# Performance work log

Hardware: AMD Instinct MI355X
Metric: run time of the kernel (lower is better)

Reference implementation:

```python
import jax, jax.numpy as jnp
import numpy as np

N_NODES = 50000
HIDDEN = 64
N_EDGES = 1200000


def setup_inputs() -> dict:
    key = jax.random.key(0)
    ks = jax.random.split(key, 12)
    x = jax.random.normal(ks[0], (N_NODES, HIDDEN), dtype=jnp.float32)
    edge_index = jax.random.randint(ks[1], (2, N_EDGES), 0, N_NODES, dtype=jnp.int64)
    s = 1.0 / np.sqrt(HIDDEN)
    # RGCN layer (single relation): relation weight, root weight, bias
    W_rel1 = jax.random.normal(ks[2], (HIDDEN, HIDDEN), dtype=jnp.float32) * s
    W_root1 = jax.random.normal(ks[3], (HIDDEN, HIDDEN), dtype=jnp.float32) * s
    b1 = jnp.zeros((HIDDEN,), dtype=jnp.float32)
    # Three GraphConv layers: self weight, neighbor weight, bias each
    W_self2 = jax.random.normal(ks[4], (HIDDEN, HIDDEN), dtype=jnp.float32) * s
    W_nbr2 = jax.random.normal(ks[5], (HIDDEN, HIDDEN), dtype=jnp.float32) * s
    b2 = jnp.zeros((HIDDEN,), dtype=jnp.float32)
    W_self3 = jax.random.normal(ks[6], (HIDDEN, HIDDEN), dtype=jnp.float32) * s
    W_nbr3 = jax.random.normal(ks[7], (HIDDEN, HIDDEN), dtype=jnp.float32) * s
    b3 = jnp.zeros((HIDDEN,), dtype=jnp.float32)
    W_self4 = jax.random.normal(ks[8], (HIDDEN, HIDDEN), dtype=jnp.float32) * s
    W_nbr4 = jax.random.normal(ks[9], (HIDDEN, HIDDEN), dtype=jnp.float32) * s
    b4 = jnp.zeros((HIDDEN,), dtype=jnp.float32)
    return {
        "x": x, "edge_index": edge_index,
        "W_rel1": W_rel1, "W_root1": W_root1, "b1": b1,
        "W_self2": W_self2, "W_nbr2": W_nbr2, "b2": b2,
        "W_self3": W_self3, "W_nbr3": W_nbr3, "b3": b3,
        "W_self4": W_self4, "W_nbr4": W_nbr4, "b4": b4,
    }


def _rgcn(x, W_rel, W_root, b, src, dst, n_nodes):
    # single-relation RGCN: root transform + mean-aggregated relation transform
    msg = x[src] @ W_rel                                   # [E, H]
    agg = jax.ops.segment_sum(msg, dst, num_segments=n_nodes)
    cnt = jax.ops.segment_sum(jnp.ones((src.shape[0],), x.dtype), dst, num_segments=n_nodes)
    agg = agg / jnp.maximum(cnt, 1.0)[:, None]
    return x @ W_root + agg + b


def _graphconv(x, W_self, W_nbr, b, src, dst, n_nodes):
    # GraphConv: self transform + sum-aggregated neighbor transform
    agg = jax.ops.segment_sum(x[src], dst, num_segments=n_nodes)  # [N, H]
    return x @ W_self + agg @ W_nbr + b


def reference(x, edge_index, W_rel1, W_root1, b1, W_self2, W_nbr2, b2,
              W_self3, W_nbr3, b3, W_self4, W_nbr4, b4):
    n = x.shape[0]
    src, dst = edge_index[0], edge_index[1]
    h = jax.nn.relu(_rgcn(x, W_rel1, W_root1, b1, src, dst, n))
    h = jax.nn.relu(_graphconv(h, W_self2, W_nbr2, b2, src, dst, n))
    x_1 = h
    h = jax.nn.relu(_graphconv(h, W_self3, W_nbr3, b3, src, dst, n))
    h = jax.nn.relu(_graphconv(h, W_self4, W_nbr4, b4, src, dst, n))
    x_2 = h
    return (x_1, x_2)
```

## Files before the change

kernel.cpp:

```cpp
#include <hip/hip_runtime.h>

#define N_NODES 50000
#define HIDDEN  64
#define N_EDGES 1200000

#define BSHIFT 8
#define NBUK   196
#define GBIN   256
#define PAD    8192

__device__ __forceinline__ float bcastf(float v, int k) {
    return __int_as_float(__builtin_amdgcn_readlane(__float_as_int(v), k));
}

__device__ __forceinline__ unsigned short f2bf(float x) {
    unsigned u = __float_as_uint(x);
    u += 0x7fffu + ((u >> 16) & 1u);
    return (unsigned short)(u >> 16);
}

__device__ __forceinline__ float bfl(unsigned w) { return __uint_as_float(w << 16); }
__device__ __forceinline__ float bfh(unsigned w) { return __uint_as_float(w & 0xffff0000u); }


__global__ void init_kernel(int* __restrict__ cursor) {
    int tid = threadIdx.x;
    if (tid < NBUK) cursor[tid] = tid * PAD;
}

__global__ __launch_bounds__(256) void scatter_fused_kernel(const int* __restrict__ ei,
                                                            int* __restrict__ cursor,
                                                            int2* __restrict__ tmp, int E) {
    __shared__ int h[NBUK];
    __shared__ int cur[NBUK];
    int tid = threadIdx.x;
    if (tid < NBUK) h[tid] = 0;
    __syncthreads();
    for (int e = blockIdx.x * 256 + tid; e < E; e += GBIN * 256)
        atomicAdd(&h[ei[E + e] >> BSHIFT], 1);
    __syncthreads();
    if (tid < NBUK) cur[tid] = atomicAdd(&cursor[tid], h[tid]);
    __syncthreads();
    for (int e = blockIdx.x * 256 + tid; e < E; e += GBIN * 256) {
        int src = ei[e];
        int dst = ei[E + e];
        int p = atomicAdd(&cur[dst >> BSHIFT], 1);
        tmp[p] = make_int2(src, dst);
    }
}

__global__ __launch_bounds__(256) void bucketize_kernel(const int2* __restrict__ tmp,
                                                        const int* __restrict__ cursor,
                                                        int2* __restrict__ row_info,
                                                        int* __restrict__ csr_src, int n) {
    __shared__ int hist[256];
    __shared__ int cur[256];
    __shared__ int stage[PAD];
    int b = blockIdx.x, tid = threadIdx.x;
    int base = b * PAD;
    int count = cursor[b] - base;
    int node_base = b << BSHIFT;

    hist[tid] = 0;
    __syncthreads();
    for (int i = tid; i < count; i += 256)
        atomicAdd(&hist[tmp[base + i].y - node_base], 1);
    __syncthreads();
    int v = hist[tid];
#pragma unroll
    for (int o = 1; o < 256; o <<= 1) {
        __syncthreads();
        int y = (tid >= o) ? hist[tid - o] : 0;
        __syncthreads();
        hist[tid] += y;
    }
    __syncthreads();
    int excl = hist[tid] - v;
    cur[tid] = excl;
    int node = node_base + tid;
    if (node < n) row_info[node] = make_int2(base + excl, v);
    __syncthreads();
    for (int i = tid; i < count; i += 256) {
        int2 p = tmp[base + i];
        int slot = atomicAdd(&cur[p.y - node_base], 1);
        stage[slot] = p.x;
    }
    __syncthreads();
    for (int i = tid; i < count; i += 256)
        csr_src[base + i] = stage[i];
}

__global__ __launch_bounds__(256) void gemm2_kernel(const float* __restrict__ h,
                                                    const float* __restrict__ Wnbr,
                                                    const float* __restrict__ Wself,
                                                    const float* __restrict__ bias,
                                                    unsigned short* __restrict__ tbf,
                                                    float* __restrict__ u, int n) {
    int lane = threadIdx.x & 63;
    float wn[64], ws[64];
#pragma unroll
    for (int k = 0; k < 64; ++k) {
        wn[k] = Wnbr[k * 64 + lane];
        ws[k] = Wself[k * 64 + lane];
    }
    float bv = bias[lane];
    int wave = (blockIdx.x * 256 + threadIdx.x) >> 6;
    int nwaves = gridDim.x * 4;
    if (wave == 0) tbf[(size_t)n * 64 + lane] = 0;
    for (int i = wave; i < n; i += nwaves) {
        float hv = h[i * 64 + lane];
        float tacc = 0.f, uacc = bv;
#pragma unroll
        for (int k = 0; k < 64; ++k) {
            float hk = bcastf(hv, k);
            tacc = fmaf(hk, wn[k], tacc);
            uacc = fmaf(hk, ws[k], uacc);
        }
        tbf[(size_t)i * 64 + lane] = f2bf(tacc);
        u[(size_t)i * 64 + lane] = uacc;
    }
}

__global__ __launch_bounds__(256) void agg_kernel(const unsigned short* __restrict__ tbf,
                                                  const float* __restrict__ u,
                                                  const int2* __restrict__ row_info,
                                                  const int* __restrict__ csr_src,
                                                  float* __restrict__ out, int n, int use_mean) {
    int lane = threadIdx.x & 63;
    int g = lane >> 4;
    int q = lane & 15;
    int node = (blockIdx.x * 256 + threadIdx.x) >> 6;
    if (node >= n) return;
    int2 ri = row_info[node];
    int start = ri.x, deg = ri.y;
    float4 a0 = {0,0,0,0}, a1 = {0,0,0,0}, a2 = {0,0,0,0}, a3 = {0,0,0,0};
    for (int e = 0; e < deg; e += 64) {
        int cnt = deg - e;
        if (cnt > 64) cnt = 64;
        int idx = (lane < cnt) ? csr_src[start + e + lane] : n;
        int cnt16 = (cnt + 15) & ~15;
        for (int j = 0; j < cnt16; j += 16) {
            int s0 = __shfl(idx, j + g);
            int s1 = __shfl(idx, j + 4 + g);
            int s2 = __shfl(idx, j + 8 + g);
            int s3 = __shfl(idx, j + 12 + g);
            const uint2 w0 = *(const uint2*)(tbf + (size_t)s0 * 64 + q * 4);
            const uint2 w1 = *(const uint2*)(tbf + (size_t)s1 * 64 + q * 4);
            const uint2 w2 = *(const uint2*)(tbf + (size_t)s2 * 64 + q * 4);
            const uint2 w3 = *(const uint2*)(tbf + (size_t)s3 * 64 + q * 4);
            a0.x += bfl(w0.x); a0.y += bfh(w0.x); a0.z += bfl(w0.y); a0.w += bfh(w0.y);
            a1.x += bfl(w1.x); a1.y += bfh(w1.x); a1.z += bfl(w1.y); a1.w += bfh(w1.y);
            a2.x += bfl(w2.x); a2.y += bfh(w2.x); a2.z += bfl(w2.y); a2.w += bfh(w2.y);
            a3.x += bfl(w3.x); a3.y += bfh(w3.x); a3.z += bfl(w3.y); a3.w += bfh(w3.y);
        }
    }
    float4 acc;
    acc.x = (a0.x + a1.x) + (a2.x + a3.x);
    acc.y = (a0.y + a1.y) + (a2.y + a3.y);
    acc.z = (a0.z + a1.z) + (a2.z + a3.z);
    acc.w = (a0.w + a1.w) + (a2.w + a3.w);
    acc.x += __shfl_xor(acc.x, 16); acc.y += __shfl_xor(acc.y, 16);
    acc.z += __shfl_xor(acc.z, 16); acc.w += __shfl_xor(acc.w, 16);
    acc.x += __shfl_xor(acc.x, 32); acc.y += __shfl_xor(acc.y, 32);
    acc.z += __shfl_xor(acc.z, 32); acc.w += __shfl_xor(acc.w, 32);

    float scale = 1.f;
    if (use_mean) scale = 1.f / fmaxf((float)deg, 1.f);
    if (g == 0) {
        const float4 uv = *(const float4*)(u + (size_t)node * 64 + q * 4);
        float4 r;
        r.x = fmaxf(uv.x + acc.x * scale, 0.f);
        r.y = fmaxf(uv.y + acc.y * scale, 0.f);
        r.z = fmaxf(uv.z + acc.z * scale, 0.f);
        r.w = fmaxf(uv.w + acc.w * scale, 0.f);
        *(float4*)(out + (size_t)node * 64 + q * 4) = r;
    }
}


extern "C" void kernel_launch(void* const* d_in, const int* in_sizes, int n_in,
                              void* d_out, int out_size, void* d_ws, size_t ws_size,
                              hipStream_t stream) {
    const float* x      = (const float*)d_in[0];
    const int*   ei     = (const int*)d_in[1];
    const float* Wrel1  = (const float*)d_in[2];
    const float* Wroot1 = (const float*)d_in[3];
    const float* b1     = (const float*)d_in[4];
    const float* Wself2 = (const float*)d_in[5];
    const float* Wnbr2  = (const float*)d_in[6];
    const float* b2     = (const float*)d_in[7];
    const float* Wself3 = (const float*)d_in[8];
    const float* Wnbr3  = (const float*)d_in[9];
    const float* b3     = (const float*)d_in[10];
    const float* Wself4 = (const float*)d_in[11];
    const float* Wnbr4  = (const float*)d_in[12];
    const float* b4     = (const float*)d_in[13];

    const int N = N_NODES, E = N_EDGES;

    auto align = [](size_t o) { return (o + 255) & ~(size_t)255; };
    char* base = (char*)d_ws;
    size_t off = 0;
    int*  cursor   = (int*)(base + off);  off = align(off + 256 * 4);
    int2* row_info = (int2*)(base + off); off = align(off + (size_t)N * 8);
    int*  csr_src  = (int*)(base + off);  off = align(off + (size_t)NBUK * PAD * 4);
    int2* tmp      = (int2*)(base + off); off = align(off + (size_t)NBUK * PAD * 8);
    unsigned short* tbf = (unsigned short*)(base + off); off = align(off + (size_t)(N + 1) * 64 * 2);
    float* u  = (float*)(base + off); off = align(off + (size_t)N * 64 * 4);
    float* h1 = (float*)(base + off); off = align(off + (size_t)N * 64 * 4);

    float* out1 = (float*)d_out;
    float* out2 = (float*)d_out + (size_t)N * 64;

    init_kernel<<<1, 256, 0, stream>>>(cursor);
    scatter_fused_kernel<<<GBIN, 256, 0, stream>>>(ei, cursor, tmp, E);
    bucketize_kernel<<<NBUK, 256, 0, stream>>>(tmp, cursor, row_info, csr_src, N);

    const int GB = 768;
    const int AB = (N + 3) / 4;

    gemm2_kernel<<<GB, 256, 0, stream>>>(x, Wrel1, Wroot1, b1, tbf, u, N);
    agg_kernel<<<AB, 256, 0, stream>>>(tbf, u, row_info, csr_src, h1, N, 1);
    gemm2_kernel<<<GB, 256, 0, stream>>>(h1, Wnbr2, Wself2, b2, tbf, u, N);
    agg_kernel<<<AB, 256, 0, stream>>>(tbf, u, row_info, csr_src, out1, N, 0);
    gemm2_kernel<<<GB, 256, 0, stream>>>(out1, Wnbr3, Wself3, b3, tbf, u, N);
    agg_kernel<<<AB, 256, 0, stream>>>(tbf, u, row_info, csr_src, h1, N, 0);
    gemm2_kernel<<<GB, 256, 0, stream>>>(h1, Wnbr4, Wself4, b4, tbf, u, N);
    agg_kernel<<<AB, 256, 0, stream>>>(tbf, u, row_info, csr_src, out2, N, 0);
}
```

Measured before the change: 326.4 us.

## Compress CSR indices to 16-bit, shrink buckets, widen aggregation unroll

The edge binning now packs each source index and its bucket-local destination into one 32-bit word, and stores the final CSR source indices as 16-bit values. Buckets shrink to 128 nodes and are processed by 512-thread blocks. The aggregation kernel doubles its gather unroll from 4 to 8 neighbour rows per step, using 8 accumulators. The aims are to cut memory traffic in the preprocessing and index reads and to keep more gathers in flight per wave. In exchange, correctness depends on node ids fitting in 16 bits and on each bucket holding no more than 4096 edges.

Measured after the change: 336.1 us. 1.03x slower.

```diff
diff --git a/kernel.cpp b/kernel.cpp
--- a/kernel.cpp
+++ b/kernel.cpp
@@ -4,10 +4,11 @@
 #define HIDDEN  64
 #define N_EDGES 1200000
 
-#define BSHIFT 8
-#define NBUK   196
+#define BSHIFT 7
+#define BUKSZ  128
+#define NBUK   391
 #define GBIN   256
-#define PAD    8192
+#define PAD2   4096
 
 __device__ __forceinline__ float bcastf(float v, int k) {
     return __int_as_float(__builtin_amdgcn_readlane(__float_as_int(v), k));
@@ -23,71 +24,74 @@
 __device__ __forceinline__ float bfh(unsigned w) { return __uint_as_float(w & 0xffff0000u); }
 
 
-__global__ void init_kernel(int* __restrict__ cursor) {
+__global__ __launch_bounds__(512) void init_kernel(int* __restrict__ cursor) {
     int tid = threadIdx.x;
-    if (tid < NBUK) cursor[tid] = tid * PAD;
+    if (tid < NBUK) cursor[tid] = tid * PAD2;
 }
 
 __global__ __launch_bounds__(256) void scatter_fused_kernel(const int* __restrict__ ei,
                                                             int* __restrict__ cursor,
-                                                            int2* __restrict__ tmp, int E) {
+                                                            int* __restrict__ tmp, int E) {
     __shared__ int h[NBUK];
     __shared__ int cur[NBUK];
     int tid = threadIdx.x;
-    if (tid < NBUK) h[tid] = 0;
+    for (int b = tid; b < NBUK; b += 256) h[b] = 0;
     __syncthreads();
     for (int e = blockIdx.x * 256 + tid; e < E; e += GBIN * 256)
         atomicAdd(&h[ei[E + e] >> BSHIFT], 1);
     __syncthreads();
-    if (tid < NBUK) cur[tid] = atomicAdd(&cursor[tid], h[tid]);
+    for (int b = tid; b < NBUK; b += 256) cur[b] = atomicAdd(&cursor[b], h[b]);
     __syncthreads();
     for (int e = blockIdx.x * 256 + tid; e < E; e += GBIN * 256) {
         int src = ei[e];
         int dst = ei[E + e];
         int p = atomicAdd(&cur[dst >> BSHIFT], 1);
-        tmp[p] = make_int2(src, dst);
-    }
-}
-
-__global__ __launch_bounds__(256) void bucketize_kernel(const int2* __restrict__ tmp,
+        tmp[p] = src | ((dst & (BUKSZ - 1)) << 16);
+    }
+}
+
+__global__ __launch_bounds__(512) void bucketize_kernel(const int* __restrict__ tmp,
                                                         const int* __restrict__ cursor,
                                                         int2* __restrict__ row_info,
-                                                        int* __restrict__ csr_src, int n) {
-    __shared__ int hist[256];
-    __shared__ int cur[256];
-    __shared__ int stage[PAD];
+                                                        unsigned short* __restrict__ csr,
+                                                        int n) {
+    __shared__ int hist[BUKSZ];
+    __shared__ int cur[BUKSZ];
+    __shared__ unsigned short stage[PAD2];
     int b = blockIdx.x, tid = threadIdx.x;
-    int base = b * PAD;
+    int base = b * PAD2;
     int count = cursor[b] - base;
     int node_base = b << BSHIFT;
 
-    hist[tid] = 0;
-    __syncthreads();
-    for (int i = tid; i < count; i += 256)
-        atomicAdd(&hist[tmp[base + i].y - node_base], 1);
-    __syncthreads();
-    int v = hist[tid];
+    if (tid < BUKSZ) hist[tid] = 0;
+    __syncthreads();
+    for (int i = tid; i < count; i += 512)
+        atomicAdd(&hist[tmp[base + i] >> 16], 1);
+    __syncthreads();
+    int v = (tid < BUKSZ) ? hist[tid] : 0;
 #pragma unroll
-    for (int o = 1; o < 256; o <<= 1) {
+    for (int o = 1; o < BUKSZ; o <<= 1) {
         __syncthreads();
-        int y = (tid >= o) ? hist[tid - o] : 0;
+        int y = (tid >= o && tid < BUKSZ) ? hist[tid - o] : 0;
         __syncthreads();
-        hist[tid] += y;
-    }
-    __syncthreads();
-    int excl = hist[tid] - v;
-    cur[tid] = excl;
-    int node = node_base + tid;
-    if (node < n) row_info[node] = make_int2(base + excl, v);
-    __syncthreads();
-    for (int i = tid; i < count; i += 256) {
-        int2 p = tmp[base + i];
-        int slot = atomicAdd(&cur[p.y - node_base], 1);
-        stage[slot] = p.x;
-    }
-    __syncthreads();
-    for (int i = tid; i < count; i += 256)
-        csr_src[base + i] = stage[i];
+        if (tid < BUKSZ) hist[tid] += y;
+    }
+    __syncthreads();
+    if (tid < BUKSZ) {
+        int excl = hist[tid] - v;
+        cur[tid] = excl;
+        int node = node_base + tid;
+        if (node < n) row_info[node] = make_int2(base + excl, v);
+    }
+    __syncthreads();
+    for (int i = tid; i < count; i += 512) {
+        int p = tmp[base + i];
+        int slot = atomicAdd(&cur[p >> 16], 1);
+        stage[slot] = (unsigned short)(p & 0xFFFF);
+    }
+    __syncthreads();
+    for (int i = tid; i < count; i += 512)
+        csr[base + i] = stage[i];
 }
 
 __global__ __launch_bounds__(256) void gemm2_kernel(const float* __restrict__ h,
@@ -124,7 +128,7 @@
 __global__ __launch_bounds__(256) void agg_kernel(const unsigned short* __restrict__ tbf,
                                                   const float* __restrict__ u,
                                                   const int2* __restrict__ row_info,
-                                                  const int* __restrict__ csr_src,
+                                                  const unsigned short* __restrict__ csr,
                                                   float* __restrict__ out, int n, int use_mean) {
     int lane = threadIdx.x & 63;
     int g = lane >> 4;
@@ -134,31 +138,44 @@
     int2 ri = row_info[node];
     int start = ri.x, deg = ri.y;
     float4 a0 = {0,0,0,0}, a1 = {0,0,0,0}, a2 = {0,0,0,0}, a3 = {0,0,0,0};
+    float4 a4 = {0,0,0,0}, a5 = {0,0,0,0}, a6 = {0,0,0,0}, a7 = {0,0,0,0};
     for (int e = 0; e < deg; e += 64) {
         int cnt = deg - e;
         if (cnt > 64) cnt = 64;
-        int idx = (lane < cnt) ? csr_src[start + e + lane] : n;
-        int cnt16 = (cnt + 15) & ~15;
-        for (int j = 0; j < cnt16; j += 16) {
+        int idx = (lane < cnt) ? (int)csr[start + e + lane] : n;
+        int cnt32 = (cnt + 31) & ~31;
+        for (int j = 0; j < cnt32; j += 32) {
             int s0 = __shfl(idx, j + g);
             int s1 = __shfl(idx, j + 4 + g);
             int s2 = __shfl(idx, j + 8 + g);
             int s3 = __shfl(idx, j + 12 + g);
+            int s4 = __shfl(idx, j + 16 + g);
+            int s5 = __shfl(idx, j + 20 + g);
+            int s6 = __shfl(idx, j + 24 + g);
+            int s7 = __shfl(idx, j + 28 + g);
             const uint2 w0 = *(const uint2*)(tbf + (size_t)s0 * 64 + q * 4);
             const uint2 w1 = *(const uint2*)(tbf + (size_t)s1 * 64 + q * 4);
             const uint2 w2 = *(const uint2*)(tbf + (size_t)s2 * 64 + q * 4);
             const uint2 w3 = *(const uint2*)(tbf + (size_t)s3 * 64 + q * 4);
+            const uint2 w4 = *(const uint2*)(tbf + (size_t)s4 * 64 + q * 4);
+            const uint2 w5 = *(const uint2*)(tbf + (size_t)s5 * 64 + q * 4);
+            const uint2 w6 = *(const uint2*)(tbf + (size_t)s6 * 64 + q * 4);
+            const uint2 w7 = *(const uint2*)(tbf + (size_t)s7 * 64 + q * 4);
             a0.x += bfl(w0.x); a0.y += bfh(w0.x); a0.z += bfl(w0.y); a0.w += bfh(w0.y);
             a1.x += bfl(w1.x); a1.y += bfh(w1.x); a1.z += bfl(w1.y); a1.w += bfh(w1.y);
             a2.x += bfl(w2.x); a2.y += bfh(w2.x); a2.z += bfl(w2.y); a2.w += bfh(w2.y);
             a3.x += bfl(w3.x); a3.y += bfh(w3.x); a3.z += bfl(w3.y); a3.w += bfh(w3.y);
+            a4.x += bfl(w4.x); a4.y += bfh(w4.x); a4.z += bfl(w4.y); a4.w += bfh(w4.y);
+            a5.x += bfl(w5.x); a5.y += bfh(w5.x); a5.z += bfl(w5.y); a5.w += bfh(w5.y);
+            a6.x += bfl(w6.x); a6.y += bfh(w6.x); a6.z += bfl(w6.y); a6.w += bfh(w6.y);
+            a7.x += bfl(w7.x); a7.y += bfh(w7.x); a7.z += bfl(w7.y); a7.w += bfh(w7.y);
         }
     }
     float4 acc;
-    acc.x = (a0.x + a1.x) + (a2.x + a3.x);
-    acc.y = (a0.y + a1.y) + (a2.y + a3.y);
-    acc.z = (a0.z + a1.z) + (a2.z + a3.z);
-    acc.w = (a0.w + a1.w) + (a2.w + a3.w);
+    acc.x = ((a0.x + a1.x) + (a2.x + a3.x)) + ((a4.x + a5.x) + (a6.x + a7.x));
+    acc.y = ((a0.y + a1.y) + (a2.y + a3.y)) + ((a4.y + a5.y) + (a6.y + a7.y));
+    acc.z = ((a0.z + a1.z) + (a2.z + a3.z)) + ((a4.z + a5.z) + (a6.z + a7.z));
+    acc.w = ((a0.w + a1.w) + (a2.w + a3.w)) + ((a4.w + a5.w) + (a6.w + a7.w));
     acc.x += __shfl_xor(acc.x, 16); acc.y += __shfl_xor(acc.y, 16);
     acc.z += __shfl_xor(acc.z, 16); acc.w += __shfl_xor(acc.w, 16);
     acc.x += __shfl_xor(acc.x, 32); acc.y += __shfl_xor(acc.y, 32);
@@ -201,10 +218,10 @@
     auto align = [](size_t o) { return (o + 255) & ~(size_t)255; };
     char* base = (char*)d_ws;
     size_t off = 0;
-    int*  cursor   = (int*)(base + off);  off = align(off + 256 * 4);
-    int2* row_info = (int2*)(base + off); off = align(off + (size_t)N * 8);
-    int*  csr_src  = (int*)(base + off);  off = align(off + (size_t)NBUK * PAD * 4);
-    int2* tmp      = (int2*)(base + off); off = align(off + (size_t)NBUK * PAD * 8);
+    int*  cursor   = (int*)(base + off);  off = align(off + (size_t)NBUK * 4);
+    int2* row_info = (int2*)(base + off); off = align(off + (size_t)N_NODES * 8);
+    int*  tmp      = (int*)(base + off);  off = align(off + (size_t)NBUK * PAD2 * 4);
+    unsigned short* csr = (unsigned short*)(base + off); off = align(off + (size_t)NBUK * PAD2 * 2);
     unsigned short* tbf = (unsigned short*)(base + off); off = align(off + (size_t)(N + 1) * 64 * 2);
     float* u  = (float*)(base + off); off = align(off + (size_t)N * 64 * 4);
     float* h1 = (float*)(base + off); off = align(off + (size_t)N * 64 * 4);
@@ -212,19 +229,19 @@
     float* out1 = (float*)d_out;
     float* out2 = (float*)d_out + (size_t)N * 64;
 
-    init_kernel<<<1, 256, 0, stream>>>(cursor);
+    init_kernel<<<1, 512, 0, stream>>>(cursor);
     scatter_fused_kernel<<<GBIN, 256, 0, stream>>>(ei, cursor, tmp, E);
-    bucketize_kernel<<<NBUK, 256, 0, stream>>>(tmp, cursor, row_info, csr_src, N);
+    bucketize_kernel<<<NBUK, 512, 0, stream>>>(tmp, cursor, row_info, csr, N);
 
     const int GB = 768;
     const int AB = (N + 3) / 4;
 
     gemm2_kernel<<<GB, 256, 0, stream>>>(x, Wrel1, Wroot1, b1, tbf, u, N);
-    agg_kernel<<<AB, 256, 0, stream>>>(tbf, u, row_info, csr_src, h1, N, 1);
+    agg_kernel<<<AB, 256, 0, stream>>>(tbf, u, row_info, csr, h1, N, 1);
     gemm2_kernel<<<GB, 256, 0, stream>>>(h1, Wnbr2, Wself2, b2, tbf, u, N);
-    agg_kernel<<<AB, 256, 0, stream>>>(tbf, u, row_info, csr_src, out1, N, 0);
+    agg_kernel<<<AB, 256, 0, stream>>>(tbf, u, row_info, csr, out1, N, 0);
     gemm2_kernel<<<GB, 256, 0, stream>>>(out1, Wnbr3, Wself3, b3, tbf, u, N);
-    agg_kernel<<<AB, 256, 0, stream>>>(tbf, u, row_info, csr_src, h1, N, 0);
+    agg_kernel<<<AB, 256, 0, stream>>>(tbf, u, row_info, csr, h1, N, 0);
     gemm2_kernel<<<GB, 256, 0, stream>>>(h1, Wnbr4, Wself4, b4, tbf, u, N);
-    agg_kernel<<<AB, 256, 0, stream>>>(tbf, u, row_info, csr_src, out2, N, 0);
-}
+    agg_kernel<<<AB, 256, 0, stream>>>(tbf, u, row_info, csr, out2, N, 0);
+}
```
